# Performance work log

Hardware: AMD Instinct MI355X
Metric: run time of the kernel (lower is better)

## Reference

```python
import jax, jax.numpy as jnp
import numpy as np

EPS = 0.5      # sinkhorn eps used by assign_batch_sinkhorn
NITERS = 15    # sinkhorn iterations used by assign_batch_sinkhorn


def pairwise_dists(features, centroids):
    # ||f - c|| via the expansion ||f||^2 + ||c||^2 - 2 f.c (avoids the
    # [B, nc, D] intermediate the naive broadcast would materialize).
    f2 = jnp.sum(features * features, axis=-1)          # [B]
    c2 = jnp.sum(centroids * centroids, axis=-1)        # [K]
    d2 = f2[:, None] + c2[None, :] - 2.0 * features @ centroids.T  # [B, K]
    return jnp.sqrt(jnp.maximum(d2, 0.0))


def sinkhorn(scores, eps=EPS, niters=NITERS):
    # Faithful to the torch sinkhorn(): Q = exp(scores/eps).T, normalize
    # columns (sum over K), then alternate row/column scalings.
    Q = jnp.exp(scores / eps).T                          # [K, B]
    Q = Q / jnp.sum(Q, axis=0, keepdims=True)
    K, B = Q.shape
    r = jnp.ones((K,), Q.dtype) / K
    c = jnp.ones((B,), Q.dtype) / B

    def body(_, Q):
        Q = Q * (r / jnp.sum(Q, axis=1))[:, None]
        Q = Q * (c / jnp.sum(Q, axis=0))[None, :]
        return Q

    Q = jax.lax.fori_loop(0, niters, body, Q)
    return (Q / jnp.sum(Q, axis=0, keepdims=True)).T     # [B, K]


def setup_inputs() -> dict:
    key = jax.random.key(0)
    kf, kc = jax.random.split(key)
    B, K, D = 16384, 2048, 1000
    # 0.1 scale keeps dists ~O(5) so exp(-dists/eps) stays in fp32 range
    # (unit-randn 1000-dim features give dists ~45 -> exp underflow).
    features = 0.1 * jax.random.normal(kf, (B, D), dtype=jnp.float32)
    centroids = 0.1 * jax.random.normal(kc, (K, D), dtype=jnp.float32)
    return {"features": features, "centroids": centroids}


def reference(features, centroids):
    B, K = features.shape[0], centroids.shape[0]
    dists = pairwise_dists(features, centroids)          # [B, K]

    # assign_batch_sinkhorn (soft assignments computed under no_grad)
    soft = jax.lax.stop_gradient(sinkhorn(-dists))       # [B, K]
    batch_assignments = jnp.argmin(soft, axis=1)         # [B] (as in source)
    soft_counts = jnp.sum(soft, axis=0)                  # [K]
    cluster_loss = jnp.mean(
        jnp.take_along_axis(dists, batch_assignments[:, None], axis=1))

    # the per-element python count loops, as fused scatter-adds
    cluster_counts = jnp.zeros((K,), jnp.int32).at[batch_assignments].add(1)
    raw_assign = jnp.argmin(dists, axis=1)
    raw_counts = jnp.zeros((K,), jnp.int32).at[raw_assign].add(1)

    return cluster_loss, batch_assignments, soft_counts, cluster_counts, raw_counts
```

## Files before the change

### kernel.cpp

```cpp
#include <hip/hip_runtime.h>

typedef __attribute__((ext_vector_type(8))) short bf16x8;
typedef __attribute__((ext_vector_type(4))) float f32x4;

#define NB 16384
#define NK 2048
#define ND 1000
#define KP 1024
#define NCHK 1024

__device__ float  g_dist[(size_t)NB * NK];
__device__ ushort g_E[(size_t)NB * NK];
__device__ ushort g_Fh[(size_t)NB * KP], g_Fl[(size_t)NB * KP];
__device__ ushort g_Ch[(size_t)NK * KP], g_Cl[(size_t)NK * KP];
__device__ float  g_u[NK], g_c2[NK], g_scnt[NK];
__device__ float  g_f2[NB], g_bd[NB];
__device__ float  g_part[(size_t)NCHK * NK];
__device__ int    g_cc[NK], g_rc[NK];

typedef const __attribute__((address_space(1))) void gvoid_t;
typedef __attribute__((address_space(3))) void lvoid_t;

union h16 { ushort u; _Float16 h; };

__device__ __forceinline__ ushort bf16_rne(float x){
    uint u = __float_as_uint(x);
    uint lsb = (u >> 16) & 1u;
    u += 0x7fffu + lsb;
    return (ushort)(u >> 16);
}
__device__ __forceinline__ float bf16_to_f(ushort h){
    return __uint_as_float(((uint)h) << 16);
}

template<int WHICH>
__global__ __launch_bounds__(256) void cn_prep(const float* __restrict__ X){
    ushort* __restrict__ H = WHICH ? g_Ch : g_Fh;
    ushort* __restrict__ L = WHICH ? g_Cl : g_Fl;
    float*  __restrict__ sq = WHICH ? g_c2 : g_f2;
    const int row = blockIdx.x, t = threadIdx.x;
    const int lane = t & 63, wid = t >> 6;
    float4 x = make_float4(0.f,0.f,0.f,0.f);
    if (t < 250) x = *(const float4*)(X + (size_t)row * ND + 4 * t);
    double s = (double)x.x*x.x + (double)x.y*x.y + (double)x.z*x.z + (double)x.w*x.w;
    ushort4 h4, l4;
#pragma unroll
    for (int c = 0; c < 4; ++c){
        float xc = (&x.x)[c];
        ushort h = bf16_rne(xc);
        (&h4.x)[c] = h;
        (&l4.x)[c] = bf16_rne(xc - bf16_to_f(h));
    }
    const int base = (t >> 3) << 5;
    const int grp  = (t >> 1) & 3;
    const int pos  = base + ((grp ^ ((row >> 1) & 3)) << 3) + ((4 * t) & 7);
    *(ushort4*)&H[(size_t)row * KP + pos] = h4;
    *(ushort4*)&L[(size_t)row * KP + pos] = l4;

    __shared__ double pr[4];
    for (int off = 32; off; off >>= 1) s += __shfl_xor(s, off);
    if (lane == 0) pr[wid] = s;
    __syncthreads();
    if (t == 0) sq[row] = (float)(pr[0] + pr[1] + pr[2] + pr[3]);
}

__global__ __launch_bounds__(256) void cn_gemm_dist(){
    __shared__ __attribute__((aligned(16))) ushort Ah[128 * 32];
    __shared__ __attribute__((aligned(16))) ushort Al[128 * 32];
    __shared__ __attribute__((aligned(16))) ushort Bh[128 * 32];
    __shared__ __attribute__((aligned(16))) ushort Bl[128 * 32];

    const int tid = threadIdx.x;
    const int lane = tid & 63, wid = tid >> 6;
    const int wr = wid >> 1, wc = wid & 1;
    const int brow0 = blockIdx.y * 128, bcol0 = blockIdx.x * 128;

    f32x4 acc[4][4];
#pragma unroll
    for (int m = 0; m < 4; ++m)
#pragma unroll
        for (int n = 0; n < 4; ++n) acc[m][n] = (f32x4){0.f,0.f,0.f,0.f};

    const int lrow = lane >> 2;
    const int lcol = (lane & 3) * 8;

    for (int step = 0; step < 32; ++step){
        const int k0 = step * 32;
#pragma unroll
        for (int i = 0; i < 2; ++i){
            const int ch = wid * 2 + i;
            const int ldso = ch * 512;
            const size_t ga = ((size_t)(brow0 + ch * 16 + lrow)) * KP + k0 + lcol;
            const size_t gb = ((size_t)(bcol0 + ch * 16 + lrow)) * KP + k0 + lcol;
            __builtin_amdgcn_global_load_lds((gvoid_t*)(g_Fh + ga), (lvoid_t*)(Ah + ldso), 16, 0, 0);
            __builtin_amdgcn_global_load_lds((gvoid_t*)(g_Fl + ga), (lvoid_t*)(Al + ldso), 16, 0, 0);
            __builtin_amdgcn_global_load_lds((gvoid_t*)(g_Ch + gb), (lvoid_t*)(Bh + ldso), 16, 0, 0);
            __builtin_amdgcn_global_load_lds((gvoid_t*)(g_Cl + gb), (lvoid_t*)(Bl + ldso), 16, 0, 0);
        }
        __syncthreads();

        const int arow = wr * 64 + (lane & 15);
        const int brow = wc * 64 + (lane & 15);
        const int kof  = (((lane >> 4) ^ ((lane >> 1) & 3)) * 8);
        bf16x8 afh[4], afl[4], bfh[4], bfl[4];
#pragma unroll
        for (int m = 0; m < 4; ++m){
            afh[m] = *(const bf16x8*)&Ah[(arow + m * 16) * 32 + kof];
            afl[m] = *(const bf16x8*)&Al[(arow + m * 16) * 32 + kof];
        }
#pragma unroll
        for (int n = 0; n < 4; ++n){
            bfh[n] = *(const bf16x8*)&Bh[(brow + n * 16) * 32 + kof];
            bfl[n] = *(const bf16x8*)&Bl[(brow + n * 16) * 32 + kof];
        }
#pragma unroll
        for (int m = 0; m < 4; ++m)
#pragma unroll
            for (int n = 0; n < 4; ++n){
                acc[m][n] = __builtin_amdgcn_mfma_f32_16x16x32_bf16(afh[m], bfh[n], acc[m][n], 0, 0, 0);
                acc[m][n] = __builtin_amdgcn_mfma_f32_16x16x32_bf16(afh[m], bfl[n], acc[m][n], 0, 0, 0);
                acc[m][n] = __builtin_amdgcn_mfma_f32_16x16x32_bf16(afl[m], bfh[n], acc[m][n], 0, 0, 0);
            }
        __syncthreads();
    }

#pragma unroll
    for (int m = 0; m < 4; ++m){
        int rowb = brow0 + wr * 64 + m * 16 + (lane >> 4) * 4;
#pragma unroll
        for (int n = 0; n < 4; ++n){
            int col = bcol0 + wc * 64 + n * 16 + (lane & 15);
            float c2v = g_c2[col];
#pragma unroll
            for (int j = 0; j < 4; ++j){
                float d2 = g_f2[rowb + j] + c2v - 2.0f * acc[m][n][j];
                float d  = sqrtf(fmaxf(d2, 0.0f));
                size_t idx = (size_t)(rowb + j) * NK + col;
                g_dist[idx] = d;
                h16 cv; cv.h = (_Float16)(__expf(-2.0f * d) * 8192.0f);
                g_E[idx] = cv.u;
            }
        }
    }
}

template<int MODE>
__global__ __launch_bounds__(256) void cn_sweep(float* __restrict__ outba){
    __shared__ float4 sred[3][8][64];
    const int lane = threadIdx.x & 63, wid = threadIdx.x >> 6;
    const int row0 = (blockIdx.x * 4 + wid) * 4;
    const float cst = (MODE == 0) ? 1.0f : (1.0f / (float)NB);

    float4 uu[8];
    float4 ak[8];
    if (MODE >= 1){
#pragma unroll
        for (int j = 0; j < 8; ++j)
            uu[j] = *(const float4*)&g_u[4 * lane + 256 * j];
    }
    if (MODE == 3){
#pragma unroll
        for (int j = 0; j < 8; ++j)
#pragma unroll
            for (int c = 0; c < 4; ++c)
                (&ak[j].x)[c] = (float)log((double)(&uu[j].x)[c] * (double)NK);
    }

    float4 S[8];
#pragma unroll
    for (int j = 0; j < 8; ++j) S[j] = make_float4(0.f,0.f,0.f,0.f);

    for (int r = 0; r < 4; ++r){
        const int b = row0 + r;
        float4 ev[8];
        float4 dv[8];
        float tsum = 0.f;
        if (MODE <= 1){
            const ushort* er = g_E + (size_t)b * NK + 4 * lane;
#pragma unroll
            for (int j = 0; j < 8; ++j){
                ushort4 q4 = *(const ushort4*)(er + 256 * j);
                float4 e4;
#pragma unroll
                for (int c = 0; c < 4; ++c){
                    h16 cv; cv.u = (&q4.x)[c];
                    float e = (float)cv.h;
                    (&e4.x)[c] = e;
                    tsum += (MODE == 1) ? e * (&uu[j].x)[c] : e;
                }
                ev[j] = e4;
            }
        } else {
            const float* dr = g_dist + (size_t)b * NK + 4 * lane;
#pragma unroll
            for (int j = 0; j < 8; ++j){
                float4 d4 = *(const float4*)(dr + 256 * j);
                float4 e4;
#pragma unroll
                for (int c = 0; c < 4; ++c){
                    float e = __expf(-2.0f * (&d4.x)[c]);
                    (&e4.x)[c] = e;
                    tsum += e * (&uu[j].x)[c];
                }
                ev[j] = e4;
                if (MODE == 3) dv[j] = d4;
            }
        }
#pragma unroll
        for (int off = 32; off; off >>= 1) tsum += __shfl_xor(tsum, off);
        const float v = cst / tsum;
#pragma unroll
        for (int j = 0; j < 8; ++j){
#pragma unroll
            for (int c = 0; c < 4; ++c)
                (&S[j].x)[c] += (&ev[j].x)[c] * v;
        }

        if (MODE == 3){
            double bestT = -1.0e300; int bi = 0; float bd = 0.f;
            float rbest = 3.4e38f;   int ri = 0;
#pragma unroll
            for (int j = 0; j < 8; ++j){
#pragma unroll
                for (int c = 0; c < 4; ++c){
                    int k = 256 * j + 4 * lane + c;
                    float d = (&dv[j].x)[c];
                    double t = 2.0 * (double)d - (double)(&ak[j].x)[c];
                    if (t > bestT){ bestT = t; bi = k; bd = d; }
                    if (d < rbest){ rbest = d; ri = k; }
                }
            }
            for (int off = 32; off; off >>= 1){
                double oT = __shfl_xor(bestT, off);
                int    oi = __shfl_xor(bi, off);
                float  od = __shfl_xor(bd, off);
                if (oT > bestT || (oT == bestT && oi < bi)){ bestT = oT; bi = oi; bd = od; }
                float orb = __shfl_xor(rbest, off);
                int   ori = __shfl_xor(ri, off);
                if (orb < rbest || (orb == rbest && ori < ri)){ rbest = orb; ri = ori; }
            }
            if (lane == 0){
                outba[b] = (float)bi;
                g_bd[b] = bd;
                atomicAdd(&g_cc[bi], 1);
                atomicAdd(&g_rc[ri], 1);
            }
        }
    }

    if (wid > 0){
#pragma unroll
        for (int j = 0; j < 8; ++j) sred[wid - 1][j][lane] = S[j];
    }
    __syncthreads();
    if (wid == 0){
#pragma unroll
        for (int w = 0; w < 3; ++w)
#pragma unroll
            for (int j = 0; j < 8; ++j){
                float4 o = sred[w][j][lane];
                S[j].x += o.x; S[j].y += o.y; S[j].z += o.z; S[j].w += o.w;
            }
#pragma unroll
        for (int j = 0; j < 8; ++j)
            *(float4*)&g_part[(size_t)blockIdx.x * NK + 4 * lane + 256 * j] = S[j];
    }
}

__global__ __launch_bounds__(256) void cn_red(int mode){
    __shared__ double red[4][64];
    const int lane = threadIdx.x & 63, q = threadIdx.x >> 6;
    const int k = blockIdx.x * 64 + lane;
    double s = 0.0;
    for (int ch = q * 256; ch < q * 256 + 256; ++ch)
        s += (double)g_part[(size_t)ch * NK + k];
    red[q][lane] = s;
    __syncthreads();
    if (q == 0){
        double tot = red[0][lane] + red[1][lane] + red[2][lane] + red[3][lane];
        if (mode == 0) g_u[k] = (float)((1.0 / (double)NK) / tot);
        else           g_scnt[k] = (float)((double)NB * (double)g_u[k] * tot);
    }
}

__global__ __launch_bounds__(256) void cn_zero(){
    int i = blockIdx.x * 256 + threadIdx.x;
    if (i < NK){ g_cc[i] = 0; g_rc[i] = 0; }
}

__global__ __launch_bounds__(256) void cn_finalize(float* __restrict__ out){
    int i = blockIdx.x * 256 + threadIdx.x;
    if (i < NK){
        out[1 + NB + i]            = g_scnt[i];
        out[1 + NB + NK + i]       = (float)g_cc[i];
        out[1 + NB + 2 * NK + i]   = (float)g_rc[i];
    }
    if (blockIdx.x == 0){
        __shared__ double red[4];
        int lane = threadIdx.x & 63, wid = threadIdx.x >> 6;
        double s = 0.0;
        for (int b = threadIdx.x; b < NB; b += 256) s += (double)g_bd[b];
        for (int off = 32; off; off >>= 1) s += __shfl_xor(s, off);
        if (lane == 0) red[wid] = s;
        __syncthreads();
        if (threadIdx.x == 0){
            double tot = red[0] + red[1] + red[2] + red[3];
            out[0] = (float)(tot / (double)NB);
        }
    }
}

extern "C" void kernel_launch(void* const* d_in, const int* in_sizes, int n_in,
                              void* d_out, int out_size, void* d_ws, size_t ws_size,
                              hipStream_t stream){
    const float* F  = (const float*)d_in[0];
    const float* Cn = (const float*)d_in[1];
    float* out = (float*)d_out;
    (void)d_ws; (void)ws_size;

    cn_prep<0><<<NB, 256, 0, stream>>>(F);
    cn_prep<1><<<NK, 256, 0, stream>>>(Cn);
    cn_zero<<<NK / 256, 256, 0, stream>>>();

    dim3 gg(NK / 128, NB / 128);
    cn_gemm_dist<<<gg, 256, 0, stream>>>();

    cn_sweep<0><<<NCHK, 256, 0, stream>>>(nullptr);
    cn_red<<<NK / 64, 256, 0, stream>>>(0);

    for (int it = 1; it <= 9; ++it){
        cn_sweep<1><<<NCHK, 256, 0, stream>>>(nullptr);
        cn_red<<<NK / 64, 256, 0, stream>>>(0);
    }
    for (int it = 10; it <= 14; ++it){
        cn_sweep<2><<<NCHK, 256, 0, stream>>>(nullptr);
        cn_red<<<NK / 64, 256, 0, stream>>>(0);
    }

    cn_sweep<3><<<NCHK, 256, 0, stream>>>(out + 1);
    cn_red<<<NK / 64, 256, 0, stream>>>(1);

    cn_finalize<<<NK / 256, 256, 0, stream>>>(out);
}
```

Baseline: 775.5 us.

## Widen fp16 sweep loads, parallelize column reduction, fuse zero/finalize kernels

The fp16 sweep modes now load 8 halves per lane in one 16-byte access and re-decode them instead of keeping float copies, which lowers register pressure. The column reduction is replaced by a kernel that spreads each column over 32 lanes with shuffle reduction, giving more blocks and parallelism. Zeroing of the counters moves into the centroid prep kernel, and the last reduction is merged with finalize, removing two launches. More iterations now use the cheaper fp16 E matrix (11 instead of 9) rather than recomputing exp from fp32 distances, which trades some accuracy for less memory traffic.

```diff
diff --git a/kernel.cpp b/kernel.cpp
--- a/kernel.cpp
+++ b/kernel.cpp
@@ -1,6 +1,7 @@
 #include <hip/hip_runtime.h>
 
 typedef __attribute__((ext_vector_type(8))) short bf16x8;
+typedef __attribute__((ext_vector_type(8))) unsigned short ushort8_t;
 typedef __attribute__((ext_vector_type(4))) float f32x4;
 
 #define NB 16384
@@ -13,7 +14,7 @@
 __device__ ushort g_E[(size_t)NB * NK];
 __device__ ushort g_Fh[(size_t)NB * KP], g_Fl[(size_t)NB * KP];
 __device__ ushort g_Ch[(size_t)NK * KP], g_Cl[(size_t)NK * KP];
-__device__ float  g_u[NK], g_c2[NK], g_scnt[NK];
+__device__ float  g_u[NK], g_c2[NK];
 __device__ float  g_f2[NB], g_bd[NB];
 __device__ float  g_part[(size_t)NCHK * NK];
 __device__ int    g_cc[NK], g_rc[NK];
@@ -40,6 +41,7 @@
     float*  __restrict__ sq = WHICH ? g_c2 : g_f2;
     const int row = blockIdx.x, t = threadIdx.x;
     const int lane = t & 63, wid = t >> 6;
+    if (WHICH == 1 && t == 0){ g_cc[row] = 0; g_rc[row] = 0; }
     float4 x = make_float4(0.f,0.f,0.f,0.f);
     if (t < 250) x = *(const float4*)(X + (size_t)row * ND + 4 * t);
     double s = (double)x.x*x.x + (double)x.y*x.y + (double)x.z*x.z + (double)x.w*x.w;
@@ -153,7 +155,14 @@
 
     float4 uu[8];
     float4 ak[8];
-    if (MODE >= 1){
+    if (MODE == 1){
+#pragma unroll
+        for (int j = 0; j < 4; ++j)
+#pragma unroll
+            for (int h = 0; h < 2; ++h)
+                uu[2 * j + h] = *(const float4*)&g_u[512 * j + 8 * lane + 4 * h];
+    }
+    if (MODE >= 2){
 #pragma unroll
         for (int j = 0; j < 8; ++j)
             uu[j] = *(const float4*)&g_u[4 * lane + 256 * j];
@@ -172,78 +181,82 @@
 
     for (int r = 0; r < 4; ++r){
         const int b = row0 + r;
-        float4 ev[8];
-        float4 dv[8];
         float tsum = 0.f;
         if (MODE <= 1){
-            const ushort* er = g_E + (size_t)b * NK + 4 * lane;
-#pragma unroll
-            for (int j = 0; j < 8; ++j){
-                ushort4 q4 = *(const ushort4*)(er + 256 * j);
-                float4 e4;
-#pragma unroll
-                for (int c = 0; c < 4; ++c){
-                    h16 cv; cv.u = (&q4.x)[c];
+            ushort8_t q8[4];
+            const ushort* er = g_E + (size_t)b * NK + 8 * lane;
+#pragma unroll
+            for (int j = 0; j < 4; ++j){
+                q8[j] = *(const ushort8_t*)(er + 512 * j);
+#pragma unroll
+                for (int c = 0; c < 8; ++c){
+                    h16 cv; cv.u = q8[j][c];
                     float e = (float)cv.h;
-                    (&e4.x)[c] = e;
-                    tsum += (MODE == 1) ? e * (&uu[j].x)[c] : e;
-                }
-                ev[j] = e4;
-            }
+                    tsum += (MODE == 1) ? e * (&uu[2 * j + (c >> 2)].x)[c & 3] : e;
+                }
+            }
+#pragma unroll
+            for (int off = 32; off; off >>= 1) tsum += __shfl_xor(tsum, off);
+            const float v = cst / tsum;
+#pragma unroll
+            for (int j = 0; j < 4; ++j)
+#pragma unroll
+                for (int c = 0; c < 8; ++c){
+                    h16 cv; cv.u = q8[j][c];
+                    (&S[2 * j + (c >> 2)].x)[c & 3] += (float)cv.h * v;
+                }
         } else {
+            float4 ev[8], dv[8];
             const float* dr = g_dist + (size_t)b * NK + 4 * lane;
 #pragma unroll
             for (int j = 0; j < 8; ++j){
                 float4 d4 = *(const float4*)(dr + 256 * j);
-                float4 e4;
 #pragma unroll
                 for (int c = 0; c < 4; ++c){
                     float e = __expf(-2.0f * (&d4.x)[c]);
-                    (&e4.x)[c] = e;
+                    (&ev[j].x)[c] = e;
                     tsum += e * (&uu[j].x)[c];
                 }
-                ev[j] = e4;
                 if (MODE == 3) dv[j] = d4;
             }
-        }
-#pragma unroll
-        for (int off = 32; off; off >>= 1) tsum += __shfl_xor(tsum, off);
-        const float v = cst / tsum;
-#pragma unroll
-        for (int j = 0; j < 8; ++j){
-#pragma unroll
-            for (int c = 0; c < 4; ++c)
-                (&S[j].x)[c] += (&ev[j].x)[c] * v;
-        }
-
-        if (MODE == 3){
-            double bestT = -1.0e300; int bi = 0; float bd = 0.f;
-            float rbest = 3.4e38f;   int ri = 0;
+#pragma unroll
+            for (int off = 32; off; off >>= 1) tsum += __shfl_xor(tsum, off);
+            const float v = cst / tsum;
 #pragma unroll
             for (int j = 0; j < 8; ++j){
-#pragma unroll
-                for (int c = 0; c < 4; ++c){
-                    int k = 256 * j + 4 * lane + c;
-                    float d = (&dv[j].x)[c];
-                    double t = 2.0 * (double)d - (double)(&ak[j].x)[c];
-                    if (t > bestT){ bestT = t; bi = k; bd = d; }
-                    if (d < rbest){ rbest = d; ri = k; }
-                }
-            }
-            for (int off = 32; off; off >>= 1){
-                double oT = __shfl_xor(bestT, off);
-                int    oi = __shfl_xor(bi, off);
-                float  od = __shfl_xor(bd, off);
-                if (oT > bestT || (oT == bestT && oi < bi)){ bestT = oT; bi = oi; bd = od; }
-                float orb = __shfl_xor(rbest, off);
-                int   ori = __shfl_xor(ri, off);
-                if (orb < rbest || (orb == rbest && ori < ri)){ rbest = orb; ri = ori; }
-            }
-            if (lane == 0){
-                outba[b] = (float)bi;
-                g_bd[b] = bd;
-                atomicAdd(&g_cc[bi], 1);
-                atomicAdd(&g_rc[ri], 1);
+                S[j].x += ev[j].x * v; S[j].y += ev[j].y * v;
+                S[j].z += ev[j].z * v; S[j].w += ev[j].w * v;
+            }
+
+            if (MODE == 3){
+                double bestT = -1.0e300; int bi = 0; float bd = 0.f;
+                float rbest = 3.4e38f;   int ri = 0;
+#pragma unroll
+                for (int j = 0; j < 8; ++j){
+#pragma unroll
+                    for (int c = 0; c < 4; ++c){
+                        int k = 256 * j + 4 * lane + c;
+                        float d = (&dv[j].x)[c];
+                        double t = 2.0 * (double)d - (double)(&ak[j].x)[c];
+                        if (t > bestT){ bestT = t; bi = k; bd = d; }
+                        if (d < rbest){ rbest = d; ri = k; }
+                    }
+                }
+                for (int off = 32; off; off >>= 1){
+                    double oT = __shfl_xor(bestT, off);
+                    int    oi = __shfl_xor(bi, off);
+                    float  od = __shfl_xor(bd, off);
+                    if (oT > bestT || (oT == bestT && oi < bi)){ bestT = oT; bi = oi; bd = od; }
+                    float orb = __shfl_xor(rbest, off);
+                    int   ori = __shfl_xor(ri, off);
+                    if (orb < rbest || (orb == rbest && ori < ri)){ rbest = orb; ri = ori; }
+                }
+                if (lane == 0){
+                    outba[b] = (float)bi;
+                    g_bd[b] = bd;
+                    atomicAdd(&g_cc[bi], 1);
+                    atomicAdd(&g_rc[ri], 1);
+                }
             }
         }
     }
@@ -261,14 +274,35 @@
                 float4 o = sred[w][j][lane];
                 S[j].x += o.x; S[j].y += o.y; S[j].z += o.z; S[j].w += o.w;
             }
-#pragma unroll
-        for (int j = 0; j < 8; ++j)
-            *(float4*)&g_part[(size_t)blockIdx.x * NK + 4 * lane + 256 * j] = S[j];
-    }
-}
-
-__global__ __launch_bounds__(256) void cn_red(int mode){
+        if (MODE <= 1){
+#pragma unroll
+            for (int j = 0; j < 4; ++j)
+#pragma unroll
+                for (int h = 0; h < 2; ++h)
+                    *(float4*)&g_part[(size_t)blockIdx.x * NK + 512 * j + 8 * lane + 4 * h] = S[2 * j + h];
+        } else {
+#pragma unroll
+            for (int j = 0; j < 8; ++j)
+                *(float4*)&g_part[(size_t)blockIdx.x * NK + 4 * lane + 256 * j] = S[j];
+        }
+    }
+}
+
+__global__ __launch_bounds__(256) void cn_red0(){
+    const int sub = threadIdx.x & 31;
+    const int k = blockIdx.x * 8 + (threadIdx.x >> 5);
+    double s = 0.0;
+#pragma unroll 8
+    for (int i = 0; i < 32; ++i)
+        s += (double)g_part[(size_t)(i * 32 + sub) * NK + k];
+    s += __shfl_xor(s, 16); s += __shfl_xor(s, 8);
+    s += __shfl_xor(s, 4);  s += __shfl_xor(s, 2);  s += __shfl_xor(s, 1);
+    if (sub == 0) g_u[k] = (float)((1.0 / (double)NK) / s);
+}
+
+__global__ __launch_bounds__(256) void cn_fin(float* __restrict__ out){
     __shared__ double red[4][64];
+    __shared__ double lred[4];
     const int lane = threadIdx.x & 63, q = threadIdx.x >> 6;
     const int k = blockIdx.x * 64 + lane;
     double s = 0.0;
@@ -278,35 +312,20 @@
     __syncthreads();
     if (q == 0){
         double tot = red[0][lane] + red[1][lane] + red[2][lane] + red[3][lane];
-        if (mode == 0) g_u[k] = (float)((1.0 / (double)NK) / tot);
-        else           g_scnt[k] = (float)((double)NB * (double)g_u[k] * tot);
-    }
-}
-
-__global__ __launch_bounds__(256) void cn_zero(){
-    int i = blockIdx.x * 256 + threadIdx.x;
-    if (i < NK){ g_cc[i] = 0; g_rc[i] = 0; }
-}
-
-__global__ __launch_bounds__(256) void cn_finalize(float* __restrict__ out){
-    int i = blockIdx.x * 256 + threadIdx.x;
-    if (i < NK){
-        out[1 + NB + i]            = g_scnt[i];
-        out[1 + NB + NK + i]       = (float)g_cc[i];
-        out[1 + NB + 2 * NK + i]   = (float)g_rc[i];
+        out[1 + NB + k] = (float)((double)NB * (double)g_u[k] * tot);
+    } else if (q == 1){
+        out[1 + NB + NK + k] = (float)g_cc[k];
+    } else if (q == 2){
+        out[1 + NB + 2 * NK + k] = (float)g_rc[k];
     }
     if (blockIdx.x == 0){
-        __shared__ double red[4];
-        int lane = threadIdx.x & 63, wid = threadIdx.x >> 6;
-        double s = 0.0;
-        for (int b = threadIdx.x; b < NB; b += 256) s += (double)g_bd[b];
-        for (int off = 32; off; off >>= 1) s += __shfl_xor(s, off);
-        if (lane == 0) red[wid] = s;
+        double sl = 0.0;
+        for (int b = threadIdx.x; b < NB; b += 256) sl += (double)g_bd[b];
+        for (int off = 32; off; off >>= 1) sl += __shfl_xor(sl, off);
+        if (lane == 0) lred[q] = sl;
         __syncthreads();
-        if (threadIdx.x == 0){
-            double tot = red[0] + red[1] + red[2] + red[3];
-            out[0] = (float)(tot / (double)NB);
-        }
+        if (threadIdx.x == 0)
+            out[0] = (float)((lred[0] + lred[1] + lred[2] + lred[3]) / (double)NB);
     }
 }
 
@@ -320,25 +339,20 @@
 
     cn_prep<0><<<NB, 256, 0, stream>>>(F);
     cn_prep<1><<<NK, 256, 0, stream>>>(Cn);
-    cn_zero<<<NK / 256, 256, 0, stream>>>();
 
     dim3 gg(NK / 128, NB / 128);
     cn_gemm_dist<<<gg, 256, 0, stream>>>();
 
     cn_sweep<0><<<NCHK, 256, 0, stream>>>(nullptr);
-    cn_red<<<NK / 64, 256, 0, stream>>>(0);
-
-    for (int it = 1; it <= 9; ++it){
+    cn_red0<<<NK / 8, 256, 0, stream>>>();
+    for (int it = 1; it <= 11; ++it){
         cn_sweep<1><<<NCHK, 256, 0, stream>>>(nullptr);
-        cn_red<<<NK / 64, 256, 0, stream>>>(0);
-    }
-    for (int it = 10; it <= 14; ++it){
+        cn_red0<<<NK / 8, 256, 0, stream>>>();
+    }
+    for (int it = 12; it <= 14; ++it){
         cn_sweep<2><<<NCHK, 256, 0, stream>>>(nullptr);
-        cn_red<<<NK / 64, 256, 0, stream>>>(0);
-    }
-
+        cn_red0<<<NK / 8, 256, 0, stream>>>();
+    }
     cn_sweep<3><<<NCHK, 256, 0, stream>>>(out + 1);
-    cn_red<<<NK / 64, 256, 0, stream>>>(1);
-
-    cn_finalize<<<NK / 256, 256, 0, stream>>>(out);
-}
+    cn_fin<<<NK / 64, 256, 0, stream>>>(out);
+}
```

Result: no change. 762.1 us (-1.7%).
